# Optimization experiments

Hardware: AMD Instinct MI355X
Metric: run time of the kernel (lower is better)

## Reference

```python
import jax, jax.numpy as jnp
import numpy as np

D = 256      # channels / model dim
HEADS = 8
DK = 32
DV = 32
B, H, W = 8, 32, 32
EPS = 1e-5


def setup_inputs() -> dict:
    key = jax.random.key(0)
    ks = jax.random.split(key, 9)
    s = 0.02
    return {
        "x":  jax.random.normal(ks[0], (B, D, H, W), dtype=jnp.float32),
        "Wq": jax.random.normal(ks[1], (HEADS * DK, D), dtype=jnp.float32) * s,
        "bq": jnp.zeros((HEADS * DK,), dtype=jnp.float32),
        "Wk": jax.random.normal(ks[2], (HEADS * DK, D), dtype=jnp.float32) * s,
        "bk": jnp.zeros((HEADS * DK,), dtype=jnp.float32),
        "Wv": jax.random.normal(ks[3], (HEADS * DV, D), dtype=jnp.float32) * s,
        "bv": jnp.zeros((HEADS * DV,), dtype=jnp.float32),
        "Wo": jax.random.normal(ks[4], (D, HEADS * DK), dtype=jnp.float32) * s,
        "bo": jnp.zeros((D,), dtype=jnp.float32),
    }


def reference(x, Wq, bq, Wk, bk, Wv, bv, Wo, bo):
    b, c, h, w = x.shape
    n = h * w
    # LayerNorm over [c, h, w] per sample, no affine (functional.layer_norm default)
    mu = jnp.mean(x, axis=(1, 2, 3), keepdims=True)
    var = jnp.var(x, axis=(1, 2, 3), keepdims=True)
    xn = (x - mu) * jax.lax.rsqrt(var + EPS)
    xr = xn.reshape(b, c, n).transpose(0, 2, 1)  # [b, n, c]

    def proj(Wt, bt, dh):
        y = xr @ Wt.T + bt                        # [b, n, heads*dh]
        return y.reshape(b, n, HEADS, dh).transpose(0, 2, 1, 3)  # [b, heads, n, dh]

    q = proj(Wq, bq, DK)
    k = proj(Wk, bk, DK)
    v = proj(Wv, bv, DV)

    scores = jnp.einsum('bhid,bhjd->bhij', q, k) * (DK ** -0.5)  # [b, heads, n, n]
    att = jax.nn.softmax(scores, axis=-1)
    tmp = jnp.einsum('bhij,bhjd->bhid', att, v)                  # [b, heads, n, dv]
    tmp = tmp.transpose(0, 2, 1, 3).reshape(b, n, HEADS * DV)    # [b, n, heads*dv]
    out = tmp @ Wo.T + bo                                        # [b, n, d]
    # NOTE: original does a raw .view(b, d, h, w) WITHOUT permuting — faithful reshape
    out = out.reshape(b, c, h, w)
    return out + x
```

## Files before the change

kernel.cpp:

```cpp
#include <hip/hip_runtime.h>
#include <stdint.h>

typedef unsigned short u16;
typedef unsigned int u32;
typedef __attribute__((ext_vector_type(8))) short bf16x8;
typedef __attribute__((ext_vector_type(4))) float f32x4;
typedef __attribute__((ext_vector_type(16))) float f32x16;

#define NTOK 1024
#define DMODEL 256
#define NHEAD 8
#define DK 32
#define NBATCH 8
#define PER_B (DMODEL * NTOK)

__device__ __forceinline__ float b2f(u16 h) {
    union { unsigned u; float f; } c; c.u = ((unsigned)h) << 16; return c.f;
}
__device__ __forceinline__ u16 f2b(float f) {
    unsigned u = __float_as_uint(f);
    unsigned r = u + 0x7fffu + ((u >> 16) & 1u);
    return (u16)(r >> 16);
}

__global__ void prep(const float* __restrict__ Wq, const float* __restrict__ Wk,
                     const float* __restrict__ Wv, const float* __restrict__ Wo,
                     u16* __restrict__ wb,
                     const float* __restrict__ x, float* __restrict__ part) {
    int bx = blockIdx.x;
    int t = threadIdx.x;
    if (bx < 256) {
        int m = bx >> 6;
        const float* W = (m == 0) ? Wq : (m == 1) ? Wk : (m == 2) ? Wv : Wo;
        int i = ((bx & 63) * 256 + t) * 4;
        float4 v = *(const float4*)&W[i];
        ushort4 o;
        o.x = f2b(v.x); o.y = f2b(v.y); o.z = f2b(v.z); o.w = f2b(v.w);
        *(ushort4*)&wb[m * 65536 + i] = o;
        return;
    }
    int blk = bx - 256;
    int b = blk >> 3, sl = blk & 7;
    int w = t >> 6, l = t & 63;
    const float* xb = x + (size_t)b * PER_B + sl * (PER_B / 8);
    float s = 0.f, ss = 0.f;
    for (int base = 0; base < PER_B / 8; base += 1024) {
        float4 v = *(const float4*)&xb[base + t * 4];
        s += v.x + v.y + v.z + v.w;
        ss += v.x * v.x + v.y * v.y + v.z * v.z + v.w * v.w;
    }
    for (int d = 1; d < 64; d <<= 1) {
        s += __shfl_xor(s, d, 64);
        ss += __shfl_xor(ss, d, 64);
    }
    __shared__ float red[2][4];
    if (l == 0) { red[0][w] = s; red[1][w] = ss; }
    __syncthreads();
    if (t == 0) {
        float S = red[0][0] + red[0][1] + red[0][2] + red[0][3];
        float SS = red[1][0] + red[1][1] + red[1][2] + red[1][3];
        part[(b * 8 + sl) * 2] = S;
        part[(b * 8 + sl) * 2 + 1] = SS;
    }
}

__global__ void normT(const float* __restrict__ x, const float* __restrict__ part,
                      u16* __restrict__ xn) {
    int b = blockIdx.z;
    int n0 = blockIdx.x * 32;
    int c0 = blockIdx.y * 32;
    int tx = threadIdx.x, ty = threadIdx.y;
    __shared__ float s_mu, s_rs;
    __shared__ float tile[32][33];
    if (tx == 0 && ty == 0) {
        float S = 0.f, SS = 0.f;
        for (int i = 0; i < 8; ++i) { S += part[(b * 8 + i) * 2]; SS += part[(b * 8 + i) * 2 + 1]; }
        float mu = S / (float)PER_B;
        float var = SS / (float)PER_B - mu * mu;
        s_mu = mu;
        s_rs = rsqrtf(var + 1e-5f);
    }
    __syncthreads();
    float mu = s_mu, rs = s_rs;
    const float* xb = x + (size_t)b * PER_B;
#pragma unroll
    for (int i = 0; i < 4; ++i) {
        int c = c0 + ty + i * 8;
        tile[ty + i * 8][tx] = (xb[c * NTOK + n0 + tx] - mu) * rs;
    }
    __syncthreads();
    u16* xnb = xn + (size_t)b * PER_B;
#pragma unroll
    for (int i = 0; i < 4; ++i) {
        int n = n0 + ty + i * 8;
        xnb[n * DMODEL + c0 + tx] = f2b(tile[tx][ty + i * 8]);
    }
}

__global__ __launch_bounds__(256, 4) void qkv_gemm(
    const u16* __restrict__ xn, const u16* __restrict__ wb,
    const float* __restrict__ bq, const float* __restrict__ bk,
    const float* __restrict__ bv,
    u16* __restrict__ qo, u16* __restrict__ ko, u16* __restrict__ vo) {
    int mt = blockIdx.x;
    int ot = blockIdx.y;
    int b = blockIdx.z;
    int sel = ot >> 2;
    int o0 = (ot & 3) * 64;
    const u16* W = wb + sel * 65536;

    __shared__ u16 As[2][64][40];
    __shared__ u16 Bs[2][64][40];
    int t = threadIdx.x;
    int w = t >> 6, l = t & 63;
    int lr = t >> 2;
    int lc = (t & 3) * 8;
    int qd = l >> 4, ln = l & 15;

    const u16* xb = xn + ((size_t)b * NTOK + mt * 64) * DMODEL;

    {
        uint4 a0 = *(const uint4*)&xb[lr * DMODEL + lc];
        uint4 b0 = *(const uint4*)&W[(o0 + lr) * DMODEL + lc];
        *(uint4*)&As[0][lr][lc] = a0;
        *(uint4*)&Bs[0][lr][lc] = b0;
    }
    __syncthreads();

    f32x4 acc[4] = {};
#pragma unroll
    for (int kb = 0; kb < 8; ++kb) {
        int cur = kb & 1;
        uint4 a1, b1;
        if (kb < 7) {
            a1 = *(const uint4*)&xb[lr * DMODEL + (kb + 1) * 32 + lc];
            b1 = *(const uint4*)&W[(o0 + lr) * DMODEL + (kb + 1) * 32 + lc];
        }
        bf16x8 af = *(const bf16x8*)&As[cur][w * 16 + ln][qd * 8];
#pragma unroll
        for (int ns = 0; ns < 4; ++ns) {
            bf16x8 bf = *(const bf16x8*)&Bs[cur][ns * 16 + ln][qd * 8];
            acc[ns] = __builtin_amdgcn_mfma_f32_16x16x32_bf16(af, bf, acc[ns], 0, 0, 0);
        }
        if (kb < 7) {
            *(uint4*)&As[cur ^ 1][lr][lc] = a1;
            *(uint4*)&Bs[cur ^ 1][lr][lc] = b1;
            __syncthreads();
        }
    }
    if (sel == 0) {
        const float scale = 0.25505654344884634f;
#pragma unroll
        for (int ns = 0; ns < 4; ++ns) {
            int o = o0 + ns * 16 + ln;
            float bias_f = bq[o];
            int head = o >> 5, d = o & 31;
#pragma unroll
            for (int r = 0; r < 4; ++r) {
                int n_row = mt * 64 + w * 16 + qd * 4 + r;
                float v = (acc[ns][r] + bias_f) * scale;
                qo[(((size_t)b * NHEAD + head) * NTOK + n_row) * DK + d] = f2b(v);
            }
        }
    } else if (sel == 1) {
#pragma unroll
        for (int ns = 0; ns < 4; ++ns) {
            int o = o0 + ns * 16 + ln;
            float bias_f = bk[o];
            int head = o >> 5, d = o & 31;
            int dh = d >> 4, h8 = (d >> 3) & 1, j = d & 7;
            size_t base = (size_t)(b * NHEAD + head) * 32768;
#pragma unroll
            for (int r = 0; r < 4; ++r) {
                int n_row = mt * 64 + w * 16 + qd * 4 + r;
                int c = n_row >> 5, w5 = n_row & 31;
                int kslot = (w5 & 19) | ((w5 & 4) << 1) | ((w5 & 8) >> 1);
                float v = acc[ns][r] + bias_f;
                ko[base + ((size_t)((c * 2 + dh) * 2 + h8)) * 256 + kslot * 8 + j] = f2b(v);
            }
        }
    } else {
        int n0 = mt * 64 + w * 16 + qd * 4;
        int c = n0 >> 5, w5 = n0 & 31;
        int grp = (w5 >> 4) & 1, h8 = (w5 >> 3) & 1, j = w5 & 7;
#pragma unroll
        for (int ns = 0; ns < 4; ++ns) {
            int o = o0 + ns * 16 + ln;
            float bias_f = bv[o];
            int head = o >> 5, d = o & 31;
            ushort4 pk;
            pk.x = f2b(acc[ns][0] + bias_f);
            pk.y = f2b(acc[ns][1] + bias_f);
            pk.z = f2b(acc[ns][2] + bias_f);
            pk.w = f2b(acc[ns][3] + bias_f);
            size_t base = (size_t)(b * NHEAD + head) * 32768;
            *(ushort4*)&vo[base + ((size_t)((c * 2 + grp) * 2 + h8)) * 256 + d * 8 + j] = pk;
        }
    }
}

__global__ __launch_bounds__(256, 3) void attn(
    const u16* __restrict__ qws, const u16* __restrict__ kpan,
    const u16* __restrict__ vpan, u16* __restrict__ tmp) {
    int bh = blockIdx.x;
    int qp = blockIdx.y;
    int b = bh >> 3, h = bh & 7;
    const u16* Q  = qws + (size_t)bh * NTOK * DK;
    const u16* Kp = kpan + (size_t)bh * 32768;
    const u16* Vp = vpan + (size_t)bh * 32768;

    __shared__ float xl[2][64];
    __shared__ float xo[2][64][17];

    int t = threadIdx.x;
    int w = t >> 6, l = t & 63;
    int qsub = w >> 1, khalf = w & 1;
    int l31 = l & 31, hi = l >> 5;

    int q0 = qp * 64 + qsub * 32;
    int c0 = khalf * 16;

    bf16x8 qf0 = *(const bf16x8*)&Q[(q0 + l31) * DK + hi * 8];
    bf16x8 qf1 = *(const bf16x8*)&Q[(q0 + l31) * DK + 16 + hi * 8];

    const u16* kb = Kp + (size_t)c0 * 1024 + hi * 256 + l31 * 8;
    const u16* vb = Vp + (size_t)c0 * 1024 + hi * 256 + l31 * 8;

    f32x16 oacc = {};
    float lsum = 0.f;

#pragma unroll
    for (int c = 0; c < 8; ++c) {
        bf16x8 kf0a = *(const bf16x8*)&kb[c * 1024];
        bf16x8 kf1a = *(const bf16x8*)&kb[c * 1024 + 512];
        bf16x8 vaa  = *(const bf16x8*)&vb[c * 1024];
        bf16x8 vga  = *(const bf16x8*)&vb[c * 1024 + 512];
        bf16x8 kf0b = *(const bf16x8*)&kb[(c + 8) * 1024];
        bf16x8 kf1b = *(const bf16x8*)&kb[(c + 8) * 1024 + 512];
        bf16x8 vab  = *(const bf16x8*)&vb[(c + 8) * 1024];
        bf16x8 vgb  = *(const bf16x8*)&vb[(c + 8) * 1024 + 512];

        f32x16 sA = {};
        sA = __builtin_amdgcn_mfma_f32_32x32x16_bf16(kf0a, qf0, sA, 0, 0, 0);
        sA = __builtin_amdgcn_mfma_f32_32x32x16_bf16(kf1a, qf1, sA, 0, 0, 0);
        f32x16 sB = {};
        sB = __builtin_amdgcn_mfma_f32_32x32x16_bf16(kf0b, qf0, sB, 0, 0, 0);
        sB = __builtin_amdgcn_mfma_f32_32x32x16_bf16(kf1b, qf1, sB, 0, 0, 0);

        union { u32 u[4]; bf16x8 v; } paa, pba, pab, pbb;
        float psA = 0.f, psB = 0.f;
#pragma unroll
        for (int j = 0; j < 4; ++j) {
            float a0 = __builtin_amdgcn_exp2f(sA[2 * j]);
            float a1 = __builtin_amdgcn_exp2f(sA[2 * j + 1]);
            float a2 = __builtin_amdgcn_exp2f(sA[2 * j + 8]);
            float a3 = __builtin_amdgcn_exp2f(sA[2 * j + 9]);
            psA += (a0 + a1) + (a2 + a3);
            paa.u[j] = __builtin_amdgcn_perm(__float_as_uint(a1), __float_as_uint(a0), 0x07060302u);
            pba.u[j] = __builtin_amdgcn_perm(__float_as_uint(a3), __float_as_uint(a2), 0x07060302u);
            float b0 = __builtin_amdgcn_exp2f(sB[2 * j]);
            float b1 = __builtin_amdgcn_exp2f(sB[2 * j + 1]);
            float b2 = __builtin_amdgcn_exp2f(sB[2 * j + 8]);
            float b3 = __builtin_amdgcn_exp2f(sB[2 * j + 9]);
            psB += (b0 + b1) + (b2 + b3);
            pab.u[j] = __builtin_amdgcn_perm(__float_as_uint(b1), __float_as_uint(b0), 0x07060302u);
            pbb.u[j] = __builtin_amdgcn_perm(__float_as_uint(b3), __float_as_uint(b2), 0x07060302u);
        }
        lsum += psA + psB;

        oacc = __builtin_amdgcn_mfma_f32_32x32x16_bf16(vaa, paa.v, oacc, 0, 0, 0);
        oacc = __builtin_amdgcn_mfma_f32_32x32x16_bf16(vga, pba.v, oacc, 0, 0, 0);
        oacc = __builtin_amdgcn_mfma_f32_32x32x16_bf16(vab, pab.v, oacc, 0, 0, 0);
        oacc = __builtin_amdgcn_mfma_f32_32x32x16_bf16(vgb, pbb.v, oacc, 0, 0, 0);
    }

    if (khalf == 1) {
        xl[qsub][l] = lsum;
#pragma unroll
        for (int r = 0; r < 16; ++r) xo[qsub][l][r] = oacc[r];
    }
    __syncthreads();
    if (khalf == 0) {
        lsum += xl[qsub][l];
#pragma unroll
        for (int r = 0; r < 16; ++r) oacc[r] += xo[qsub][l][r];
        lsum += __shfl_xor(lsum, 32, 64);
        float linv = 1.0f / lsum;
        int qg = q0 + l31;
        u16* op = tmp + ((size_t)b * NTOK + qg) * DMODEL + h * DK;
#pragma unroll
        for (int g = 0; g < 4; ++g) {
            ushort4 pk;
            pk.x = f2b(oacc[g * 4 + 0] * linv);
            pk.y = f2b(oacc[g * 4 + 1] * linv);
            pk.z = f2b(oacc[g * 4 + 2] * linv);
            pk.w = f2b(oacc[g * 4 + 3] * linv);
            *(ushort4*)&op[g * 8 + hi * 4] = pk;
        }
    }
}

__global__ __launch_bounds__(256, 4) void oproj(
    const u16* __restrict__ tmp, const u16* __restrict__ wb,
    const float* __restrict__ bo, const float* __restrict__ x,
    float* __restrict__ out) {
    int mt = blockIdx.x;
    int ot = blockIdx.y;
    int b = blockIdx.z;
    const u16* Wo = wb + 3 * 65536;

    __shared__ u16 As[2][64][40];
    __shared__ u16 Bs[2][64][40];
    int t = threadIdx.x;
    int w = t >> 6, l = t & 63;
    int lr = t >> 2;
    int lc = (t & 3) * 8;
    int qd = l >> 4, ln = l & 15;

    const u16* ab = tmp + ((size_t)b * NTOK + mt * 64) * DMODEL;

    {
        uint4 a0 = *(const uint4*)&ab[lr * DMODEL + lc];
        uint4 b0 = *(const uint4*)&Wo[(ot * 64 + lr) * DMODEL + lc];
        *(uint4*)&As[0][lr][lc] = a0;
        *(uint4*)&Bs[0][lr][lc] = b0;
    }
    __syncthreads();

    f32x4 acc[4] = {};
#pragma unroll
    for (int kb = 0; kb < 8; ++kb) {
        int cur = kb & 1;
        uint4 a1, b1;
        if (kb < 7) {
            a1 = *(const uint4*)&ab[lr * DMODEL + (kb + 1) * 32 + lc];
            b1 = *(const uint4*)&Wo[(ot * 64 + lr) * DMODEL + (kb + 1) * 32 + lc];
        }
        bf16x8 af = *(const bf16x8*)&As[cur][w * 16 + ln][qd * 8];
#pragma unroll
        for (int ns = 0; ns < 4; ++ns) {
            bf16x8 bf = *(const bf16x8*)&Bs[cur][ns * 16 + ln][qd * 8];
            acc[ns] = __builtin_amdgcn_mfma_f32_16x16x32_bf16(af, bf, acc[ns], 0, 0, 0);
        }
        if (kb < 7) {
            *(uint4*)&As[cur ^ 1][lr][lc] = a1;
            *(uint4*)&Bs[cur ^ 1][lr][lc] = b1;
            __syncthreads();
        }
    }
    const float* xb = x + (size_t)b * PER_B;
    float* ob = out + (size_t)b * PER_B;
#pragma unroll
    for (int ns = 0; ns < 4; ++ns) {
        int o = ot * 64 + ns * 16 + ln;
        float bias_f = bo[o];
#pragma unroll
        for (int r = 0; r < 4; ++r) {
            int n_row = mt * 64 + w * 16 + qd * 4 + r;
            size_t idx = (size_t)n_row * DMODEL + o;
            ob[idx] = acc[ns][r] + bias_f + xb[idx];
        }
    }
}

extern "C" void kernel_launch(void* const* d_in, const int* in_sizes, int n_in,
                              void* d_out, int out_size, void* d_ws, size_t ws_size,
                              hipStream_t stream) {
    const float* x  = (const float*)d_in[0];
    const float* Wq = (const float*)d_in[1];
    const float* bq = (const float*)d_in[2];
    const float* Wk = (const float*)d_in[3];
    const float* bk = (const float*)d_in[4];
    const float* Wv = (const float*)d_in[5];
    const float* bv = (const float*)d_in[6];
    const float* Wo = (const float*)d_in[7];
    const float* bo = (const float*)d_in[8];
    float* out = (float*)d_out;

    char* ws = (char*)d_ws;
    float* part = (float*)ws;
    u16* wb  = (u16*)(ws + 1024);
    u16* xn  = (u16*)(ws + 1024 + (512u << 10));
    u16* qws = (u16*)(ws + 1024 + (512u << 10) + (4u << 20));
    u16* kws = (u16*)(ws + 1024 + (512u << 10) + (8u << 20));
    u16* vws = (u16*)(ws + 1024 + (512u << 10) + (12u << 20));
    u16* tmp = xn;

    hipLaunchKernelGGL(prep, dim3(320), dim3(256), 0, stream, Wq, Wk, Wv, Wo, wb, x, part);
    hipLaunchKernelGGL(normT, dim3(32, 8, 8), dim3(32, 8), 0, stream, x, part, xn);
    hipLaunchKernelGGL(qkv_gemm, dim3(16, 12, 8), dim3(256), 0, stream,
                       xn, wb, bq, bk, bv, qws, kws, vws);
    hipLaunchKernelGGL(attn, dim3(64, 16), dim3(256), 0, stream, qws, kws, vws, tmp);
    hipLaunchKernelGGL(oproj, dim3(16, 4, 8), dim3(256), 0, stream, tmp, wb, bo, x, out);
}
```

Baseline: 113.4 us.

## Fuse layernorm and transpose into QKV GEMM A-tile loading

Removes the separate normT kernel and has qkv_gemm read fp32 x directly, normalize it with per-batch stats from the partial sums, and transpose it into the bf16 A tile in shared memory. This drops one launch and the write/read round trip of the normalized bf16 activations. In exchange, each QKV block (12 output tiles per token tile) rereads fp32 x, doubling bytes per element and multiplying reads. It also replaces vector LDS stores with scalar 16-bit transposed stores that may bank-conflict.

```diff
diff --git a/kernel.cpp b/kernel.cpp
--- a/kernel.cpp
+++ b/kernel.cpp
@@ -64,41 +64,9 @@
     }
 }
 
-__global__ void normT(const float* __restrict__ x, const float* __restrict__ part,
-                      u16* __restrict__ xn) {
-    int b = blockIdx.z;
-    int n0 = blockIdx.x * 32;
-    int c0 = blockIdx.y * 32;
-    int tx = threadIdx.x, ty = threadIdx.y;
-    __shared__ float s_mu, s_rs;
-    __shared__ float tile[32][33];
-    if (tx == 0 && ty == 0) {
-        float S = 0.f, SS = 0.f;
-        for (int i = 0; i < 8; ++i) { S += part[(b * 8 + i) * 2]; SS += part[(b * 8 + i) * 2 + 1]; }
-        float mu = S / (float)PER_B;
-        float var = SS / (float)PER_B - mu * mu;
-        s_mu = mu;
-        s_rs = rsqrtf(var + 1e-5f);
-    }
-    __syncthreads();
-    float mu = s_mu, rs = s_rs;
-    const float* xb = x + (size_t)b * PER_B;
-#pragma unroll
-    for (int i = 0; i < 4; ++i) {
-        int c = c0 + ty + i * 8;
-        tile[ty + i * 8][tx] = (xb[c * NTOK + n0 + tx] - mu) * rs;
-    }
-    __syncthreads();
-    u16* xnb = xn + (size_t)b * PER_B;
-#pragma unroll
-    for (int i = 0; i < 4; ++i) {
-        int n = n0 + ty + i * 8;
-        xnb[n * DMODEL + c0 + tx] = f2b(tile[tx][ty + i * 8]);
-    }
-}
-
 __global__ __launch_bounds__(256, 4) void qkv_gemm(
-    const u16* __restrict__ xn, const u16* __restrict__ wb,
+    const float* __restrict__ x, const float* __restrict__ part,
+    const u16* __restrict__ wb,
     const float* __restrict__ bq, const float* __restrict__ bk,
     const float* __restrict__ bv,
     u16* __restrict__ qo, u16* __restrict__ ko, u16* __restrict__ vo) {
@@ -117,13 +85,30 @@
     int lc = (t & 3) * 8;
     int qd = l >> 4, ln = l & 15;
 
-    const u16* xb = xn + ((size_t)b * NTOK + mt * 64) * DMODEL;
+    float S = 0.f, SS = 0.f;
+#pragma unroll
+    for (int i = 0; i < 8; ++i) {
+        S  += part[(b * 8 + i) * 2];
+        SS += part[(b * 8 + i) * 2 + 1];
+    }
+    float mu = S / (float)PER_B;
+    float rs = rsqrtf(SS / (float)PER_B - mu * mu + 1e-5f);
+
+    int cq = t >> 3, n8 = t & 7;
+    const float* xb = x + (size_t)b * PER_B + (size_t)cq * NTOK + mt * 64 + n8 * 8;
 
     {
-        uint4 a0 = *(const uint4*)&xb[lr * DMODEL + lc];
-        uint4 b0 = *(const uint4*)&W[(o0 + lr) * DMODEL + lc];
-        *(uint4*)&As[0][lr][lc] = a0;
-        *(uint4*)&Bs[0][lr][lc] = b0;
+        float4 v0 = *(const float4*)&xb[0];
+        float4 v1 = *(const float4*)&xb[4];
+        As[0][n8 * 8 + 0][cq] = f2b((v0.x - mu) * rs);
+        As[0][n8 * 8 + 1][cq] = f2b((v0.y - mu) * rs);
+        As[0][n8 * 8 + 2][cq] = f2b((v0.z - mu) * rs);
+        As[0][n8 * 8 + 3][cq] = f2b((v0.w - mu) * rs);
+        As[0][n8 * 8 + 4][cq] = f2b((v1.x - mu) * rs);
+        As[0][n8 * 8 + 5][cq] = f2b((v1.y - mu) * rs);
+        As[0][n8 * 8 + 6][cq] = f2b((v1.z - mu) * rs);
+        As[0][n8 * 8 + 7][cq] = f2b((v1.w - mu) * rs);
+        *(uint4*)&Bs[0][lr][lc] = *(const uint4*)&W[(o0 + lr) * DMODEL + lc];
     }
     __syncthreads();
 
@@ -131,9 +116,12 @@
 #pragma unroll
     for (int kb = 0; kb < 8; ++kb) {
         int cur = kb & 1;
-        uint4 a1, b1;
+        float4 a0, a1;
+        uint4 b1;
         if (kb < 7) {
-            a1 = *(const uint4*)&xb[lr * DMODEL + (kb + 1) * 32 + lc];
+            const float* xn2 = xb + (size_t)(kb + 1) * 32 * NTOK;
+            a0 = *(const float4*)&xn2[0];
+            a1 = *(const float4*)&xn2[4];
             b1 = *(const uint4*)&W[(o0 + lr) * DMODEL + (kb + 1) * 32 + lc];
         }
         bf16x8 af = *(const bf16x8*)&As[cur][w * 16 + ln][qd * 8];
@@ -143,8 +131,16 @@
             acc[ns] = __builtin_amdgcn_mfma_f32_16x16x32_bf16(af, bf, acc[ns], 0, 0, 0);
         }
         if (kb < 7) {
-            *(uint4*)&As[cur ^ 1][lr][lc] = a1;
-            *(uint4*)&Bs[cur ^ 1][lr][lc] = b1;
+            int nb = cur ^ 1;
+            As[nb][n8 * 8 + 0][cq] = f2b((a0.x - mu) * rs);
+            As[nb][n8 * 8 + 1][cq] = f2b((a0.y - mu) * rs);
+            As[nb][n8 * 8 + 2][cq] = f2b((a0.z - mu) * rs);
+            As[nb][n8 * 8 + 3][cq] = f2b((a0.w - mu) * rs);
+            As[nb][n8 * 8 + 4][cq] = f2b((a1.x - mu) * rs);
+            As[nb][n8 * 8 + 5][cq] = f2b((a1.y - mu) * rs);
+            As[nb][n8 * 8 + 6][cq] = f2b((a1.z - mu) * rs);
+            As[nb][n8 * 8 + 7][cq] = f2b((a1.w - mu) * rs);
+            *(uint4*)&Bs[nb][lr][lc] = b1;
             __syncthreads();
         }
     }
@@ -380,16 +376,14 @@
     char* ws = (char*)d_ws;
     float* part = (float*)ws;
     u16* wb  = (u16*)(ws + 1024);
-    u16* xn  = (u16*)(ws + 1024 + (512u << 10));
+    u16* tmp = (u16*)(ws + 1024 + (512u << 10));
     u16* qws = (u16*)(ws + 1024 + (512u << 10) + (4u << 20));
     u16* kws = (u16*)(ws + 1024 + (512u << 10) + (8u << 20));
     u16* vws = (u16*)(ws + 1024 + (512u << 10) + (12u << 20));
-    u16* tmp = xn;
 
     hipLaunchKernelGGL(prep, dim3(320), dim3(256), 0, stream, Wq, Wk, Wv, Wo, wb, x, part);
-    hipLaunchKernelGGL(normT, dim3(32, 8, 8), dim3(32, 8), 0, stream, x, part, xn);
     hipLaunchKernelGGL(qkv_gemm, dim3(16, 12, 8), dim3(256), 0, stream,
-                       xn, wb, bq, bk, bv, qws, kws, vws);
+                       x, part, wb, bq, bk, bv, qws, kws, vws);
     hipLaunchKernelGGL(attn, dim3(64, 16), dim3(256), 0, stream, qws, kws, vws, tmp);
     hipLaunchKernelGGL(oproj, dim3(16, 4, 8), dim3(256), 0, stream, tmp, wb, bo, x, out);
 }
```

After: 118.2 us. +4.2%, slower.
